# Optimization experiments

Measured on AMD Instinct MI355X. Metric: run time of the kernel, lower is better.

## Reference

```python
import jax, jax.numpy as jnp
import numpy as np
from jax import lax

EPS = 1e-8  # torch CosineSimilarity eps


def setup_inputs() -> dict:
    key = jax.random.key(0)
    k1, k2, k3 = jax.random.split(key, 3)
    B, T, D, K = 16, 2048, 768, 64
    inputs = jax.random.normal(k1, (B, T, D), dtype=jnp.float32)
    labels = jax.random.randint(k2, (B, T), 0, K, dtype=jnp.int64)
    class_avgs = jax.random.normal(k3, (K, D), dtype=jnp.float32)
    return {"inputs": inputs, "labels": labels, "class_avgs": class_avgs}


def _simrel(inputs, labels, class_avgs):
    B, T, D = inputs.shape
    K = class_avgs.shape[0]
    vecs = inputs.reshape(B * T, D)
    labs = labels.reshape(B * T)
    class_ids = jnp.arange(K)

    def step(carry, xl):
        avgs, counts = carry  # [K,D], [K]
        vec, lab = xl  # [D], scalar int
        is_inf = jnp.any(jnp.isinf(avgs), axis=1)  # [K] unseen-class flag
        vn = jnp.maximum(jnp.linalg.norm(vec), EPS)
        an = jnp.maximum(jnp.linalg.norm(avgs, axis=1), EPS)  # [K]
        cos = (avgs @ vec) / (an * vn)  # [K]
        onehot = class_ids == lab
        # unseen class: sim = 1 (cos(vec,vec)) if labeled, else -1
        sim = jnp.where(is_inf, jnp.where(onehot, 1.0, -1.0), cos)
        # training update: running mean of labeled class (counts reset per forward)
        cnt = counts[lab]
        new_row = jnp.where(is_inf[lab], vec, (avgs[lab] * cnt + vec) / (cnt + 1.0))
        avgs = avgs.at[lab].set(new_row)
        counts = counts.at[lab].add(1.0)
        return (avgs, counts), sim

    init = (class_avgs, jnp.zeros((K,), dtype=inputs.dtype))
    (_, _), sims = lax.scan(step, init, (vecs, labs))
    return sims.reshape(B, T, K)


def reference(inputs, labels, class_avgs):
    return _simrel(inputs, labels, class_avgs)
```

## Files before the change

kernel.cpp:

```cpp
#include <hip/hip_runtime.h>
#include <cstddef>

#define K 64
#define D 768
#define D4 192

__device__ __forceinline__ float d4f(float4 a, float4 b) {
  return a.x*b.x + a.y*b.y + a.z*b.z + a.w*b.w;
}
__device__ __forceinline__ float4 a4(float4 a, float4 b) {
  return make_float4(a.x+b.x, a.y+b.y, a.z+b.z, a.w+b.w);
}
__device__ __forceinline__ unsigned short f2bf(float x) {
  unsigned int u = __float_as_uint(x);
  unsigned int r = (u + 0x7FFFu + ((u >> 16) & 1u)) >> 16;
  return (unsigned short)r;
}
__device__ __forceinline__ float bflo(unsigned u) { return __uint_as_float(u << 16); }
__device__ __forceinline__ float bfhi(unsigned u) { return __uint_as_float(u & 0xFFFF0000u); }

typedef __attribute__((ext_vector_type(8)))  short bf16x8;
typedef __attribute__((ext_vector_type(16))) float f32x16;

#define NCF 256
#define CF  128
#define NF  32768

#define LDT3 68
#define LDM  136
__global__ __launch_bounds__(256) void k2_v11(
    const float* __restrict__ inputs, const int* __restrict__ labels,
    const float* __restrict__ cavg, unsigned short* __restrict__ cavgb,
    float* __restrict__ cn2,
    unsigned short* __restrict__ sums, int* __restrict__ cnts_t)
{
  __shared__ unsigned short Vt[128 * LDT3];
  __shared__ unsigned short Mt[64 * LDM];
  __shared__ int hist[64];
  const int bi = blockIdx.x;
  const int tid = threadIdx.x;

  if (bi >= NCF * 12) {
    int wave = (bi - NCF * 12) * 4 + (tid >> 6);
    int l = tid & 63;
    if (wave >= K) return;
    const float* src = cavg + (size_t)wave * D;
    unsigned short* dst = cavgb + (size_t)wave * D;
    float sq = 0.f;
#pragma unroll
    for (int t = 0; t < 3; ++t) {
      float4 v = ((const float4*)src)[t * 64 + l];
      sq += v.x*v.x + v.y*v.y + v.z*v.z + v.w*v.w;
      ushort4 o; o.x = f2bf(v.x); o.y = f2bf(v.y); o.z = f2bf(v.z); o.w = f2bf(v.w);
      ((ushort4*)dst)[t * 64 + l] = o;
    }
#pragma unroll
    for (int mm = 1; mm <= 32; mm <<= 1) sq += __shfl_xor(sq, mm);
    if (l == 0) cn2[wave] = sq;
    return;
  }

  const int m = bi / 12, g = bi % 12;
  const int w = tid >> 6, l = tid & 63;
  const int r31 = l & 31, kh = l >> 5;
  const int ch = w & 1;
  const int cw = w >> 1;

  float4 fr[8];
#pragma unroll
  for (int it = 0; it < 8; ++it) {
    int flat = it * 256 + tid;
    int row = flat >> 4, c4 = flat & 15;
    fr[it] = *(const float4*)(inputs + (size_t)(m * 128 + row) * D + g * 64 + c4 * 4);
  }

  for (int e = tid; e < 64 * LDM / 2; e += 256) ((unsigned int*)Mt)[e] = 0u;
  if (tid < 64) hist[tid] = 0;
  __syncthreads();
  if (tid < 128) {
    int lab = labels[m * 128 + tid];
    Mt[lab * LDM + tid] = 0x3F80;
    if (g == 0) atomicAdd(&hist[lab], 1);
  }
  __syncthreads();
  if (g == 0 && tid < 64) cnts_t[tid * NCF + m] = hist[tid];

#pragma unroll
  for (int it = 0; it < 8; ++it) {
    int flat = it * 256 + tid;
    int row = flat >> 4, c4 = flat & 15;
    ushort4 o;
    o.x = f2bf(fr[it].x); o.y = f2bf(fr[it].y);
    o.z = f2bf(fr[it].z); o.w = f2bf(fr[it].w);
    *(ushort4*)(Vt + row * LDT3 + c4 * 4) = o;
  }
  __syncthreads();

  f32x16 acc = (f32x16){};
#pragma unroll
  for (int kk = 0; kk < 8; ++kk) {
    bf16x8 a = *(const bf16x8*)(Mt + (ch * 32 + r31) * LDM + kk * 16 + kh * 8);
    bf16x8 b;
#pragma unroll
    for (int r = 0; r < 8; ++r)
      b[r] = *(const short*)(Vt + (kk * 16 + kh * 8 + r) * LDT3 + cw * 32 + r31);
    acc = __builtin_amdgcn_mfma_f32_32x32x16_bf16(a, b, acc, 0, 0, 0);
  }

  __syncthreads();
  unsigned short* So = Vt;
#pragma unroll
  for (int q = 0; q < 16; ++q) {
    int kc = (q & 3) + 8 * (q >> 2) + 4 * kh;
    So[(ch * 32 + kc) * 64 + cw * 32 + r31] = f2bf(acc[q]);
  }
  __syncthreads();
  unsigned short* sp = sums + (size_t)m * (K * D) + g * 64;
#pragma unroll
  for (int it = 0; it < 2; ++it) {
    int flat = it * 256 + tid;
    int row = flat >> 3, c = flat & 7;
    *(uint4*)(sp + (size_t)row * D + c * 8) = *(const uint4*)(So + row * 64 + c * 8);
  }
}

__global__ __launch_bounds__(256) void k3a_scan_lo(
    unsigned short* __restrict__ sums, float* __restrict__ aux)
{
  const int g  = blockIdx.x / 96;
  const int cp = (blockIdx.x % 96) * 256 + threadIdx.x;
  const int col = cp * 2;
  float run0 = 0.f, run1 = 0.f;
  for (int m = g * 16; m < g * 16 + 16; ++m) {
    size_t idx = (size_t)m * (K * D) + col;
    unsigned u = *(const unsigned*)(sums + idx);
    float t0 = bflo(u), t1 = bfhi(u);
    *(unsigned*)(sums + idx) = (unsigned)f2bf(run0) | ((unsigned)f2bf(run1) << 16);
    run0 += t0; run1 += t1;
  }
  aux[(size_t)g * (K * D) + col]     = run0;
  aux[(size_t)g * (K * D) + col + 1] = run1;
}

__global__ __launch_bounds__(256) void k3b_plus(
    float* __restrict__ aux, int* __restrict__ cnts_t)
{
  if (blockIdx.x == 192) {
    if (threadIdx.x < K) {
      int k = threadIdx.x;
      int run = 0;
      int* p = cnts_t + k * NCF;
      for (int mm = 0; mm < NCF; ++mm) { int t = p[mm]; p[mm] = run; run += t; }
    }
    return;
  }
  int col = blockIdx.x * 256 + threadIdx.x;
  float run = 0.f;
  for (int g = 0; g < 16; ++g) {
    size_t idx = (size_t)g * (K * D) + col;
    float t = aux[idx]; aux[idx] = run; run += t;
  }
}

#define LDV2 136
#define LDD  132
#define BUFW (2 * 128 * LDV2)
__global__ __launch_bounds__(1024, 4) void k4_v8(
    const float* __restrict__ inputs, const unsigned short* __restrict__ base,
    const float* __restrict__ aux, const unsigned short* __restrict__ cavgb,
    const int* __restrict__ labels, const int* __restrict__ cnts_t,
    const float* __restrict__ cn2, float* __restrict__ out)
{
  __shared__ unsigned short smem[2 * BUFW];
  __shared__ float pvL[128];
  __shared__ float bn2L[64];
  __shared__ int   labL[128];
  __shared__ float segA[16][64];
  __shared__ float segF[16][64];
  __shared__ float segP[16][64];
  __shared__ int   segH[16][64];
  const int m = blockIdx.x;
  const int g = m >> 4;
  const int tid = threadIdx.x;
  const int w = tid >> 6, l = tid & 63;
  const int r31 = l & 31, kh = l >> 5;
  const int wr = w & 3;
  const int wc = w >> 2;

  if (tid < 128) labL[tid] = labels[m * 128 + tid];
  if (tid < 64) bn2L[tid] = 0.f;
  __syncthreads();

  f32x16 accP = (f32x16){}, accS = (f32x16){};

  float4 vregf[4];
  uint4 breg, creg;
  float4 areg[2];

#define PREF(sx) do {                                                          \
    _Pragma("unroll")                                                          \
    for (int it = 0; it < 4; ++it) {                                           \
      int flat = it * 1024 + tid;                                              \
      int row = flat >> 5, c4 = flat & 31;                                     \
      vregf[it] = *(const float4*)(inputs + (size_t)(m * 128 + row) * D + (sx) * 128 + c4 * 4); \
    }                                                                          \
    _Pragma("unroll")                                                          \
    for (int it = 0; it < 2; ++it) {                                           \
      int flat = it * 1024 + tid;                                              \
      int row = flat >> 4, c = flat & 15;                                      \
      if (it == 0) {                                                           \
        breg = *(const uint4*)(base + ((size_t)m * K + row) * D + (sx) * 128 + c * 8); \
        const float* ap = aux + ((size_t)g * K + row) * D + (sx) * 128 + c * 8; \
        areg[0] = *(const float4*)ap;                                          \
        areg[1] = *(const float4*)(ap + 4);                                    \
      } else {                                                                 \
        creg = *(const uint4*)(cavgb + (size_t)(row - 64) * D + (sx) * 128 + c * 8); \
      }                                                                        \
    }                                                                          \
  } while (0)

#define WRITEB(pb) do {                                                        \
    unsigned short* Vt_ = smem + (pb) * BUFW;                                  \
    unsigned short* Bt_ = Vt_ + 128 * LDV2;                                    \
    _Pragma("unroll")                                                          \
    for (int it = 0; it < 4; ++it) {                                           \
      int flat = it * 1024 + tid;                                              \
      int row = flat >> 5, c4 = flat & 31;                                     \
      ushort4 o;                                                               \
      o.x = f2bf(vregf[it].x); o.y = f2bf(vregf[it].y);                        \
      o.z = f2bf(vregf[it].z); o.w = f2bf(vregf[it].w);                        \
      *(ushort4*)(Vt_ + row * LDV2 + c4 * 4) = o;                              \
    }                                                                          \
    _Pragma("unroll")                                                          \
    for (int it = 0; it < 2; ++it) {                                           \
      int flat = it * 1024 + tid;                                              \
      int row = flat >> 4, c = flat & 15;                                      \
      if (it == 0) {                                                           \
        uint4 ub = breg;                                                       \
        float4 af0 = areg[0], af1 = areg[1];                                   \
        float f0 = bflo(ub.x) + af0.x, f1 = bfhi(ub.x) + af0.y;                \
        float f2 = bflo(ub.y) + af0.z, f3 = bfhi(ub.y) + af0.w;                \
        float f4 = bflo(ub.z) + af1.x, f5 = bfhi(ub.z) + af1.y;                \
        float f6 = bflo(ub.w) + af1.z, f7 = bfhi(ub.w) + af1.w;                \
        float sq = f0*f0 + f1*f1 + f2*f2 + f3*f3 + f4*f4 + f5*f5 + f6*f6 + f7*f7; \
        sq += __shfl_xor(sq, 1); sq += __shfl_xor(sq, 2);                      \
        sq += __shfl_xor(sq, 4); sq += __shfl_xor(sq, 8);                      \
        if ((l & 15) == 0) atomicAdd(&bn2L[row], sq);                          \
        uint4 u;                                                               \
        u.x = (unsigned)f2bf(f0) | ((unsigned)f2bf(f1) << 16);                 \
        u.y = (unsigned)f2bf(f2) | ((unsigned)f2bf(f3) << 16);                 \
        u.z = (unsigned)f2bf(f4) | ((unsigned)f2bf(f5) << 16);                 \
        u.w = (unsigned)f2bf(f6) | ((unsigned)f2bf(f7) << 16);                 \
        *(uint4*)(Bt_ + row * LDV2 + c * 8) = u;                               \
      } else {                                                                 \
        *(uint4*)(Bt_ + row * LDV2 + c * 8) = creg;                            \
      }                                                                        \
    }                                                                          \
  } while (0)

  PREF(0);
  WRITEB(0);
  PREF(1);
  __syncthreads();

  for (int s = 0; s < 6; ++s) {
    const int pb = s & 1;
    if (s < 5) WRITEB(pb ^ 1);
    if (s < 4) PREF(s + 2);
    const unsigned short* Vt = smem + pb * BUFW;
    const unsigned short* Bt = Vt + 128 * LDV2;
#pragma unroll
    for (int kk = 0; kk < 8; ++kk) {
      bf16x8 av = *(const bf16x8*)(Vt + (32 * wr + r31) * LDV2 + kk * 16 + kh * 8);
      bf16x8 bB = *(const bf16x8*)(Bt + (32 * wc + r31) * LDV2 + kk * 16 + kh * 8);
      accP = __builtin_amdgcn_mfma_f32_32x32x16_bf16(av, bB, accP, 0, 0, 0);
      if (wc <= wr) {
        bf16x8 bV = *(const bf16x8*)(Vt + (32 * wc + r31) * LDV2 + kk * 16 + kh * 8);
        accS = __builtin_amdgcn_mfma_f32_32x32x16_bf16(av, bV, accS, 0, 0, 0);
      }
    }
    __syncthreads();
  }
#undef PREF
#undef WRITEB

  if (wr == wc && ((r31 >> 2) & 1) == kh) {
    int q = (r31 & 3) + 4 * (r31 >> 3);
    pvL[32 * wr + r31] = accS[q];
  }

  {
    unsigned short* Vt = smem;
    unsigned short* Bt = smem + 128 * LDV2;
#pragma unroll
    for (int q = 0; q < 16; ++q) {
      int i = 32 * wr + (q & 3) + 8 * (q >> 2) + 4 * kh;
      int j = 32 * wc + r31;
      Vt[i * LDV2 + j] = (j < i) ? f2bf(accS[q]) : (unsigned short)0;
    }
    int j = tid & 127;
    int lab = labL[j];
    int kb = (tid >> 7) * 8;
#pragma unroll
    for (int kk = 0; kk < 8; ++kk) {
      int k = kb + kk;
      Bt[k * LDV2 + j] = (lab == k) ? (unsigned short)0x3F80 : (unsigned short)0;
    }
  }
  __syncthreads();

  if (w < 8) {
    const unsigned short* Vt = smem;
    const unsigned short* Bt = smem + 128 * LDV2;
#pragma unroll
    for (int kk = 0; kk < 8; ++kk) {
      bf16x8 aS = *(const bf16x8*)(Vt + (32 * wr + r31) * LDV2 + kk * 16 + kh * 8);
      bf16x8 bM = *(const bf16x8*)(Bt + (32 * wc + r31) * LDV2 + kk * 16 + kh * 8);
      accP = __builtin_amdgcn_mfma_f32_32x32x16_bf16(aS, bM, accP, 0, 0, 0);
    }
  }
  __syncthreads();

  float* dotL = (float*)smem;
#pragma unroll
  for (int q = 0; q < 16; ++q) {
    int i = 32 * wr + (q & 3) + 8 * (q >> 2) + 4 * kh;
    dotL[i * LDD + 32 * wc + r31] = accP[q];
  }
  __syncthreads();

  {
    int k = l;
    float A = 0.f, Fv = 0.f, Pv = 0.f;
    int has = 0;
    int jb = w * 8;
    for (int j = jb; j < jb + 8; ++j) {
      if (labL[j] == k) {
        float t = 2.f * dotL[j * LDD + k] + pvL[j];
        A += t;
        if (!has) { Fv = t; Pv = pvL[j]; has = 1; }
      }
    }
    segA[w][k] = A; segF[w][k] = Fv; segP[w][k] = Pv; segH[w][k] = has;
  }
  __syncthreads();

  {
    int k = l;
    bool seen = cnts_t[k * NCF + m] > 0;
    float n = seen ? bn2L[k] : 0.f;
    for (int ww = 0; ww < w; ++ww) {
      if (segH[ww][k]) {
        n = seen ? (n + segA[ww][k])
                 : (segP[ww][k] + segA[ww][k] - segF[ww][k]);
        seen = true;
      }
    }
    float cnk = cn2[k];
    int jb = w * 8;
    for (int j = jb; j < jb + 8; ++j) {
      float dS = dotL[j * LDD + k];
      float dC = dotL[j * LDD + 64 + k];
      float pvj = pvL[j];
      int lab = labL[j];
      float val = seen ? dS : dC;
      float nn  = seen ? n : cnk;
      out[(size_t)(m * 128 + j) * K + k] = val * rsqrtf(fmaxf(nn * pvj, 1e-30f));
      if (lab == k) {
        n = seen ? (n + 2.f * dS + pvj) : pvj;
        seen = true;
      }
    }
  }
}

__global__ __launch_bounds__(256) void ph1_chunk_sums(
    const float* __restrict__ inputs, const int* __restrict__ labels,
    float* __restrict__ sums, int* __restrict__ cnts, int NC, int C)
{
  __shared__ float acc[4 * K * 64];
  __shared__ int   hist[4 * K];
  const int bi    = blockIdx.x;
  const int chunk = bi / 12, slice = bi % 12;
  const int w = threadIdx.x >> 6, l = threadIdx.x & 63;

  for (int e = threadIdx.x; e < 4 * K * 64; e += 256) acc[e] = 0.f;
  hist[threadIdx.x] = 0;
  __syncthreads();

  const int C4 = C >> 2;
  const long long rbase = (long long)chunk * C + (long long)w * C4;
  float* accw = acc + w * (K * 64);
  for (int j = 0; j < C4; ++j) {
    long long r = rbase + j;
    int lab = labels[r];
    float v = inputs[r * D + slice * 64 + l];
    accw[lab * 64 + l] += v;
    if (slice == 0 && l == 0) hist[w * K + lab]++;
  }
  __syncthreads();

  float* sp = sums + (long long)chunk * (K * D) + slice * 64;
  for (int e = threadIdx.x; e < K * 64; e += 256) {
    int k = e >> 6, dl = e & 63;
    float s = acc[0*K*64 + e] + acc[1*K*64 + e] + acc[2*K*64 + e] + acc[3*K*64 + e];
    sp[k * D + dl] = s;
  }
  if (slice == 0 && threadIdx.x < K) {
    cnts[chunk * K + threadIdx.x] =
        hist[0*K + threadIdx.x] + hist[1*K + threadIdx.x] +
        hist[2*K + threadIdx.x] + hist[3*K + threadIdx.x];
  }
}

__global__ __launch_bounds__(256) void ph2a_scan_sums(float* __restrict__ sums, int NC)
{
  const int tid = blockIdx.x * 256 + threadIdx.x;
  float run = 0.f;
  for (int m = 0; m < NC; ++m) {
    long long idx = (long long)m * (K * D) + tid;
    float t = sums[idx];
    sums[idx] = run;
    run += t;
  }
}

__global__ void ph2b_scan_cnts(int* __restrict__ cnts, int NC)
{
  const int k = threadIdx.x;
  int run = 0;
  for (int m = 0; m < NC; ++m) {
    int t = cnts[m * K + k];
    cnts[m * K + k] = run;
    run += t;
  }
}

__global__ __launch_bounds__(256, 4) void ph3_scan(
    const float* __restrict__ inputs, const int* __restrict__ labels,
    const float* __restrict__ cavg, const float* __restrict__ base,
    const int* __restrict__ cnts, float* __restrict__ out, int NC, int C)
{
  const int bi = blockIdx.x;
  int chunk, quad;
  if (NC >= 8) {
    int xcd = bi & 7, slot = bi >> 3;
    chunk = xcd * (NC >> 3) + (slot >> 2);
    quad  = slot & 3;
  } else {
    chunk = bi >> 2; quad = bi & 3;
  }
  const int w = threadIdx.x >> 6, l = threadIdx.x & 63;
  const int k0 = (quad * 4 + w) * 4;

  const int cb = chunk * K + k0;
  bool vg0 = (cnts[cb+0] == 0), vg1 = (cnts[cb+1] == 0);
  bool vg2 = (cnts[cb+2] == 0), vg3 = (cnts[cb+3] == 0);

  const float4* bp = (const float4*)base + (long long)chunk * (K * D4);
  const float4* cp = (const float4*)cavg;

  float4 A0[3], A1[3], A2[3], A3[3];
#pragma unroll
  for (int t = 0; t < 3; ++t) {
    int o = t * 64 + l;
    A0[t] = vg0 ? cp[(k0+0)*D4 + o] : bp[(k0+0)*D4 + o];
    A1[t] = vg1 ? cp[(k0+1)*D4 + o] : bp[(k0+1)*D4 + o];
    A2[t] = vg2 ? cp[(k0+2)*D4 + o] : bp[(k0+2)*D4 + o];
    A3[t] = vg3 ? cp[(k0+3)*D4 + o] : bp[(k0+3)*D4 + o];
  }
  float n0 = 0.f, n1 = 0.f, n2 = 0.f, n3 = 0.f;
#pragma unroll
  for (int t = 0; t < 3; ++t) {
    n0 += d4f(A0[t], A0[t]); n1 += d4f(A1[t], A1[t]);
    n2 += d4f(A2[t], A2[t]); n3 += d4f(A3[t], A3[t]);
  }
#pragma unroll
  for (int m = 1; m <= 32; m <<= 1) {
    n0 += __shfl_xor(n0, m); n1 += __shfl_xor(n1, m);
    n2 += __shfl_xor(n2, m); n3 += __shfl_xor(n3, m);
  }

  const long long ibase = (long long)chunk * C;
  for (int j = 0; j < C; ++j) {
    const long long i = ibase + j;
    const int lab = labels[i];
    const float4* vp = (const float4*)inputs + i * D4;
    float4 v0 = vp[l], v1 = vp[64 + l], v2 = vp[128 + l];

    float p0 = d4f(A0[0], v0) + d4f(A0[1], v1) + d4f(A0[2], v2);
    float p1 = d4f(A1[0], v0) + d4f(A1[1], v1) + d4f(A1[2], v2);
    float p2 = d4f(A2[0], v0) + d4f(A2[1], v1) + d4f(A2[2], v2);
    float p3 = d4f(A3[0], v0) + d4f(A3[1], v1) + d4f(A3[2], v2);
    float pv = d4f(v0, v0) + d4f(v1, v1) + d4f(v2, v2);
#pragma unroll
    for (int m = 1; m <= 32; m <<= 1) {
      p0 += __shfl_xor(p0, m); p1 += __shfl_xor(p1, m);
      p2 += __shfl_xor(p2, m); p3 += __shfl_xor(p3, m);
      pv += __shfl_xor(pv, m);
    }
    if (l < 4) {
      float ps = (l == 0) ? p0 : (l == 1) ? p1 : (l == 2) ? p2 : p3;
      float ns = (l == 0) ? n0 : (l == 1) ? n1 : (l == 2) ? n2 : n3;
      out[i * K + k0 + l] = ps * rsqrtf(fmaxf(ns * pv, 1e-30f));
    }
#define UPD(idx) do { \
      if (vg##idx) { A##idx[0]=v0; A##idx[1]=v1; A##idx[2]=v2; n##idx = pv; vg##idx = false; } \
      else { A##idx[0]=a4(A##idx[0],v0); A##idx[1]=a4(A##idx[1],v1); A##idx[2]=a4(A##idx[2],v2); \
             n##idx += 2.f * p##idx + pv; } } while (0)
    if      (lab == k0 + 0) UPD(0);
    else if (lab == k0 + 1) UPD(1);
    else if (lab == k0 + 2) UPD(2);
    else if (lab == k0 + 3) UPD(3);
#undef UPD
  }
}

extern "C" void kernel_launch(void* const* d_in, const int* in_sizes, int n_in,
                              void* d_out, int out_size, void* d_ws, size_t ws_size,
                              hipStream_t stream)
{
  const float* inputs = (const float*)d_in[0];
  const int*   labels = (const int*)d_in[1];
  const float* cavg   = (const float*)d_in[2];
  float* out = (float*)d_out;
  const int N = in_sizes[1];

  const size_t szSums  = (size_t)NCF * K * D * 2;
  const size_t szAux   = (size_t)16 * K * D * 4;
  const size_t szCnt   = (size_t)K * NCF * 4;
  const size_t szCavgb = (size_t)K * D * 2;
  const size_t szCn2   = (size_t)K * 4;
  size_t need = szSums + szAux + szCnt + szCavgb + szCn2 + 8 * 256;

  if (N == NF && in_sizes[2] == K * D && ws_size >= need) {
    char* p = (char*)d_ws;
    auto take = [&](size_t b) { char* r = p; p += (b + 255) & ~(size_t)255; return r; };
    unsigned short* sums  = (unsigned short*)take(szSums);
    float*          aux   = (float*)take(szAux);
    int*            cnts  = (int*)take(szCnt);
    unsigned short* cavgb = (unsigned short*)take(szCavgb);
    float*          cn2   = (float*)take(szCn2);

    hipLaunchKernelGGL(k2_v11, dim3(NCF * 12 + 16), dim3(256), 0, stream,
                       inputs, labels, cavg, cavgb, cn2, sums, cnts);
    hipLaunchKernelGGL(k3a_scan_lo, dim3(16 * 96), dim3(256), 0, stream, sums, aux);
    hipLaunchKernelGGL(k3b_plus, dim3(193), dim3(256), 0, stream, aux, cnts);
    hipLaunchKernelGGL(k4_v8, dim3(NCF), dim3(1024), 0, stream,
                       inputs, sums, aux, cavgb, labels, cnts, cn2, out);
    return;
  }

  int NC = 256;
  while (NC > 1) {
    size_t nd = (size_t)NC * K * D * 4 + (size_t)NC * K * 4;
    if (nd <= ws_size && (N % (NC * 4)) == 0) break;
    NC >>= 1;
  }
  const int C = N / NC;
  float* d_sums = (float*)d_ws;
  int*   d_cnts = (int*)((char*)d_ws + (size_t)NC * K * D * 4);

  hipLaunchKernelGGL(ph1_chunk_sums, dim3(NC * 12), dim3(256), 0, stream,
                     inputs, labels, d_sums, d_cnts, NC, C);
  hipLaunchKernelGGL(ph2a_scan_sums, dim3((K * D) / 256), dim3(256), 0, stream,
                     d_sums, NC);
  hipLaunchKernelGGL(ph2b_scan_cnts, dim3(1), dim3(64), 0, stream,
                     d_cnts, NC);
  hipLaunchKernelGGL(ph3_scan, dim3(NC * 4), dim3(256), 0, stream,
                     inputs, labels, cavg, d_sums, d_cnts, out, NC, C);
}
```

Baseline: 72.71 us.

## Split fused GEMM+epilogue kernel into two-half GEMM blocks and separate epilogue

```diff
diff --git a/kernel.cpp b/kernel.cpp
--- a/kernel.cpp
+++ b/kernel.cpp
@@ -163,15 +163,162 @@
 }
 
 #define LDV2 136
-#define LDD  132
-#define BUFW (2 * 128 * LDV2)
-__global__ __launch_bounds__(1024, 4) void k4_v8(
+#define LDS2 136
+__global__ __launch_bounds__(512, 4) void k4a_gemm(
     const float* __restrict__ inputs, const unsigned short* __restrict__ base,
     const float* __restrict__ aux, const unsigned short* __restrict__ cavgb,
-    const int* __restrict__ labels, const int* __restrict__ cnts_t,
-    const float* __restrict__ cn2, float* __restrict__ out)
-{
-  __shared__ unsigned short smem[2 * BUFW];
+    const int* __restrict__ labels,
+    float* __restrict__ dotb, float* __restrict__ pvb, float* __restrict__ bn2b)
+{
+  __shared__ unsigned short smem[2 * 128 * LDV2];
+  __shared__ float bn2L[64];
+  __shared__ int   labL[128];
+  unsigned short* Vt = smem;
+  unsigned short* Bt = smem + 128 * LDV2;
+  const int bi = blockIdx.x;
+  const int m = bi >> 1, h = bi & 1;
+  const int g = m >> 4;
+  const int tid = threadIdx.x;
+  const int w = tid >> 6, l = tid & 63;
+  const int r31 = l & 31, kh = l >> 5;
+  const int wrg = 2 * h + (w & 1);
+  const int wc  = w >> 1;
+
+  if (tid < 128) labL[tid] = labels[m * 128 + tid];
+  if (tid < 64) bn2L[tid] = 0.f;
+
+  f32x16 accP = (f32x16){}, accS = (f32x16){};
+
+  float4 vregf[8];
+  uint4 breg[2], creg[2];
+  float4 areg[4];
+
+#define PREF(sx) do {                                                          \
+    _Pragma("unroll")                                                          \
+    for (int it = 0; it < 8; ++it) {                                           \
+      int flat = it * 512 + tid;                                               \
+      int row = flat >> 5, c4 = flat & 31;                                     \
+      vregf[it] = *(const float4*)(inputs + (size_t)(m * 128 + row) * D + (sx) * 128 + c4 * 4); \
+    }                                                                          \
+    _Pragma("unroll")                                                          \
+    for (int it = 0; it < 2; ++it) {                                           \
+      int flat = it * 512 + tid;                                               \
+      int row = flat >> 4, c = flat & 15;                                      \
+      breg[it] = *(const uint4*)(base + ((size_t)m * K + row) * D + (sx) * 128 + c * 8); \
+      const float* ap = aux + ((size_t)g * K + row) * D + (sx) * 128 + c * 8;  \
+      areg[it * 2]     = *(const float4*)ap;                                   \
+      areg[it * 2 + 1] = *(const float4*)(ap + 4);                             \
+      creg[it] = *(const uint4*)(cavgb + (size_t)row * D + (sx) * 128 + c * 8);\
+    }                                                                          \
+  } while (0)
+
+#define WRITEB() do {                                                          \
+    _Pragma("unroll")                                                          \
+    for (int it = 0; it < 8; ++it) {                                           \
+      int flat = it * 512 + tid;                                               \
+      int row = flat >> 5, c4 = flat & 31;                                     \
+      ushort4 o;                                                               \
+      o.x = f2bf(vregf[it].x); o.y = f2bf(vregf[it].y);                        \
+      o.z = f2bf(vregf[it].z); o.w = f2bf(vregf[it].w);                        \
+      *(ushort4*)(Vt + row * LDV2 + c4 * 4) = o;                               \
+    }                                                                          \
+    _Pragma("unroll")                                                          \
+    for (int it = 0; it < 2; ++it) {                                           \
+      int flat = it * 512 + tid;                                               \
+      int row = flat >> 4, c = flat & 15;                                      \
+      uint4 ub = breg[it];                                                     \
+      float4 af0 = areg[it * 2], af1 = areg[it * 2 + 1];                       \
+      float f0 = bflo(ub.x) + af0.x, f1 = bfhi(ub.x) + af0.y;                  \
+      float f2 = bflo(ub.y) + af0.z, f3 = bfhi(ub.y) + af0.w;                  \
+      float f4 = bflo(ub.z) + af1.x, f5 = bfhi(ub.z) + af1.y;                  \
+      float f6 = bflo(ub.w) + af1.z, f7 = bfhi(ub.w) + af1.w;                  \
+      float sq = f0*f0 + f1*f1 + f2*f2 + f3*f3 + f4*f4 + f5*f5 + f6*f6 + f7*f7;\
+      sq += __shfl_xor(sq, 1); sq += __shfl_xor(sq, 2);                        \
+      sq += __shfl_xor(sq, 4); sq += __shfl_xor(sq, 8);                        \
+      if ((l & 15) == 0) atomicAdd(&bn2L[row], sq);                            \
+      uint4 u;                                                                 \
+      u.x = (unsigned)f2bf(f0) | ((unsigned)f2bf(f1) << 16);                   \
+      u.y = (unsigned)f2bf(f2) | ((unsigned)f2bf(f3) << 16);                   \
+      u.z = (unsigned)f2bf(f4) | ((unsigned)f2bf(f5) << 16);                   \
+      u.w = (unsigned)f2bf(f6) | ((unsigned)f2bf(f7) << 16);                   \
+      *(uint4*)(Bt + row * LDV2 + c * 8) = u;                                  \
+      *(uint4*)(Bt + (64 + row) * LDV2 + c * 8) = creg[it];                    \
+    }                                                                          \
+  } while (0)
+
+  PREF(0);
+
+  for (int s = 0; s < 6; ++s) {
+    __syncthreads();
+    WRITEB();
+    if (s < 5) PREF(s + 1);
+    __syncthreads();
+#pragma unroll
+    for (int kk = 0; kk < 8; ++kk) {
+      bf16x8 av = *(const bf16x8*)(Vt + (32 * wrg + r31) * LDV2 + kk * 16 + kh * 8);
+      bf16x8 bB = *(const bf16x8*)(Bt + (32 * wc + r31) * LDV2 + kk * 16 + kh * 8);
+      accP = __builtin_amdgcn_mfma_f32_32x32x16_bf16(av, bB, accP, 0, 0, 0);
+      if (wc <= wrg) {
+        bf16x8 bV = *(const bf16x8*)(Vt + (32 * wc + r31) * LDV2 + kk * 16 + kh * 8);
+        accS = __builtin_amdgcn_mfma_f32_32x32x16_bf16(av, bV, accS, 0, 0, 0);
+      }
+    }
+  }
+#undef PREF
+#undef WRITEB
+
+  if (wc == wrg && ((r31 >> 2) & 1) == kh) {
+    int q = (r31 & 3) + 4 * (r31 >> 3);
+    pvb[(size_t)m * 128 + 32 * wrg + r31] = accS[q];
+  }
+  __syncthreads();
+  if (h == 0 && tid < 64) bn2b[m * 64 + tid] = bn2L[tid];
+
+  unsigned short* SL  = smem;
+  unsigned short* MtL = smem + 64 * LDS2;
+  __syncthreads();
+#pragma unroll
+  for (int q = 0; q < 16; ++q) {
+    int i_loc = 32 * (w & 1) + (q & 3) + 8 * (q >> 2) + 4 * kh;
+    int i_glob = 64 * h + i_loc;
+    int j = 32 * wc + r31;
+    SL[i_loc * LDS2 + j] = (j < i_glob) ? f2bf(accS[q]) : (unsigned short)0;
+  }
+  {
+    int j = tid & 127;
+    int lab = labL[j];
+    int kb = (tid >> 7) * 16;
+#pragma unroll
+    for (int kk = 0; kk < 16; ++kk) {
+      int k = kb + kk;
+      MtL[k * LDS2 + j] = (lab == k) ? (unsigned short)0x3F80 : (unsigned short)0;
+    }
+  }
+  __syncthreads();
+
+  if (w < 4) {
+#pragma unroll
+    for (int kk = 0; kk < 8; ++kk) {
+      bf16x8 aS = *(const bf16x8*)(SL + (32 * (w & 1) + r31) * LDS2 + kk * 16 + kh * 8);
+      bf16x8 bM = *(const bf16x8*)(MtL + (32 * (w >> 1) + r31) * LDS2 + kk * 16 + kh * 8);
+      accP = __builtin_amdgcn_mfma_f32_32x32x16_bf16(aS, bM, accP, 0, 0, 0);
+    }
+  }
+
+#pragma unroll
+  for (int q = 0; q < 16; ++q) {
+    int i_glob = 32 * wrg + (q & 3) + 8 * (q >> 2) + 4 * kh;
+    int col = 32 * wc + r31;
+    dotb[((size_t)m * 128 + i_glob) * 128 + col] = accP[q];
+  }
+}
+
+__global__ __launch_bounds__(1024) void k5_ep(
+    const float* __restrict__ dotb, const float* __restrict__ pvb,
+    const float* __restrict__ bn2b, const int* __restrict__ labels,
+    const int* __restrict__ cnts_t, const float* __restrict__ cn2,
+    float* __restrict__ out)
+{
   __shared__ float pvL[128];
   __shared__ float bn2L[64];
   __shared__ int   labL[128];
@@ -180,154 +327,14 @@
   __shared__ float segP[16][64];
   __shared__ int   segH[16][64];
   const int m = blockIdx.x;
-  const int g = m >> 4;
   const int tid = threadIdx.x;
   const int w = tid >> 6, l = tid & 63;
-  const int r31 = l & 31, kh = l >> 5;
-  const int wr = w & 3;
-  const int wc = w >> 2;
-
-  if (tid < 128) labL[tid] = labels[m * 128 + tid];
-  if (tid < 64) bn2L[tid] = 0.f;
-  __syncthreads();
-
-  f32x16 accP = (f32x16){}, accS = (f32x16){};
-
-  float4 vregf[4];
-  uint4 breg, creg;
-  float4 areg[2];
-
-#define PREF(sx) do {                                                          \
-    _Pragma("unroll")                                                          \
-    for (int it = 0; it < 4; ++it) {                                           \
-      int flat = it * 1024 + tid;                                              \
-      int row = flat >> 5, c4 = flat & 31;                                     \
-      vregf[it] = *(const float4*)(inputs + (size_t)(m * 128 + row) * D + (sx) * 128 + c4 * 4); \
-    }                                                                          \
-    _Pragma("unroll")                                                          \
-    for (int it = 0; it < 2; ++it) {                                           \
-      int flat = it * 1024 + tid;                                              \
-      int row = flat >> 4, c = flat & 15;                                      \
-      if (it == 0) {                                                           \
-        breg = *(const uint4*)(base + ((size_t)m * K + row) * D + (sx) * 128 + c * 8); \
-        const float* ap = aux + ((size_t)g * K + row) * D + (sx) * 128 + c * 8; \
-        areg[0] = *(const float4*)ap;                                          \
-        areg[1] = *(const float4*)(ap + 4);                                    \
-      } else {                                                                 \
-        creg = *(const uint4*)(cavgb + (size_t)(row - 64) * D + (sx) * 128 + c * 8); \
-      }                                                                        \
-    }                                                                          \
-  } while (0)
-
-#define WRITEB(pb) do {                                                        \
-    unsigned short* Vt_ = smem + (pb) * BUFW;                                  \
-    unsigned short* Bt_ = Vt_ + 128 * LDV2;                                    \
-    _Pragma("unroll")                                                          \
-    for (int it = 0; it < 4; ++it) {                                           \
-      int flat = it * 1024 + tid;                                              \
-      int row = flat >> 5, c4 = flat & 31;                                     \
-      ushort4 o;                                                               \
-      o.x = f2bf(vregf[it].x); o.y = f2bf(vregf[it].y);                        \
-      o.z = f2bf(vregf[it].z); o.w = f2bf(vregf[it].w);                        \
-      *(ushort4*)(Vt_ + row * LDV2 + c4 * 4) = o;                              \
-    }                                                                          \
-    _Pragma("unroll")                                                          \
-    for (int it = 0; it < 2; ++it) {                                           \
-      int flat = it * 1024 + tid;                                              \
-      int row = flat >> 4, c = flat & 15;                                      \
-      if (it == 0) {                                                           \
-        uint4 ub = breg;                                                       \
-        float4 af0 = areg[0], af1 = areg[1];                                   \
-        float f0 = bflo(ub.x) + af0.x, f1 = bfhi(ub.x) + af0.y;                \
-        float f2 = bflo(ub.y) + af0.z, f3 = bfhi(ub.y) + af0.w;                \
-        float f4 = bflo(ub.z) + af1.x, f5 = bfhi(ub.z) + af1.y;                \
-        float f6 = bflo(ub.w) + af1.z, f7 = bfhi(ub.w) + af1.w;                \
-        float sq = f0*f0 + f1*f1 + f2*f2 + f3*f3 + f4*f4 + f5*f5 + f6*f6 + f7*f7; \
-        sq += __shfl_xor(sq, 1); sq += __shfl_xor(sq, 2);                      \
-        sq += __shfl_xor(sq, 4); sq += __shfl_xor(sq, 8);                      \
-        if ((l & 15) == 0) atomicAdd(&bn2L[row], sq);                          \
-        uint4 u;                                                               \
-        u.x = (unsigned)f2bf(f0) | ((unsigned)f2bf(f1) << 16);                 \
-        u.y = (unsigned)f2bf(f2) | ((unsigned)f2bf(f3) << 16);                 \
-        u.z = (unsigned)f2bf(f4) | ((unsigned)f2bf(f5) << 16);                 \
-        u.w = (unsigned)f2bf(f6) | ((unsigned)f2bf(f7) << 16);                 \
-        *(uint4*)(Bt_ + row * LDV2 + c * 8) = u;                               \
-      } else {                                                                 \
-        *(uint4*)(Bt_ + row * LDV2 + c * 8) = creg;                            \
-      }                                                                        \
-    }                                                                          \
-  } while (0)
-
-  PREF(0);
-  WRITEB(0);
-  PREF(1);
-  __syncthreads();
-
-  for (int s = 0; s < 6; ++s) {
-    const int pb = s & 1;
-    if (s < 5) WRITEB(pb ^ 1);
-    if (s < 4) PREF(s + 2);
-    const unsigned short* Vt = smem + pb * BUFW;
-    const unsigned short* Bt = Vt + 128 * LDV2;
-#pragma unroll
-    for (int kk = 0; kk < 8; ++kk) {
-      bf16x8 av = *(const bf16x8*)(Vt + (32 * wr + r31) * LDV2 + kk * 16 + kh * 8);
-      bf16x8 bB = *(const bf16x8*)(Bt + (32 * wc + r31) * LDV2 + kk * 16 + kh * 8);
-      accP = __builtin_amdgcn_mfma_f32_32x32x16_bf16(av, bB, accP, 0, 0, 0);
-      if (wc <= wr) {
-        bf16x8 bV = *(const bf16x8*)(Vt + (32 * wc + r31) * LDV2 + kk * 16 + kh * 8);
-        accS = __builtin_amdgcn_mfma_f32_32x32x16_bf16(av, bV, accS, 0, 0, 0);
-      }
-    }
-    __syncthreads();
-  }
-#undef PREF
-#undef WRITEB
-
-  if (wr == wc && ((r31 >> 2) & 1) == kh) {
-    int q = (r31 & 3) + 4 * (r31 >> 3);
-    pvL[32 * wr + r31] = accS[q];
-  }
-
-  {
-    unsigned short* Vt = smem;
-    unsigned short* Bt = smem + 128 * LDV2;
-#pragma unroll
-    for (int q = 0; q < 16; ++q) {
-      int i = 32 * wr + (q & 3) + 8 * (q >> 2) + 4 * kh;
-      int j = 32 * wc + r31;
-      Vt[i * LDV2 + j] = (j < i) ? f2bf(accS[q]) : (unsigned short)0;
-    }
-    int j = tid & 127;
-    int lab = labL[j];
-    int kb = (tid >> 7) * 8;
-#pragma unroll
-    for (int kk = 0; kk < 8; ++kk) {
-      int k = kb + kk;
-      Bt[k * LDV2 + j] = (lab == k) ? (unsigned short)0x3F80 : (unsigned short)0;
-    }
-  }
-  __syncthreads();
-
-  if (w < 8) {
-    const unsigned short* Vt = smem;
-    const unsigned short* Bt = smem + 128 * LDV2;
-#pragma unroll
-    for (int kk = 0; kk < 8; ++kk) {
-      bf16x8 aS = *(const bf16x8*)(Vt + (32 * wr + r31) * LDV2 + kk * 16 + kh * 8);
-      bf16x8 bM = *(const bf16x8*)(Bt + (32 * wc + r31) * LDV2 + kk * 16 + kh * 8);
-      accP = __builtin_amdgcn_mfma_f32_32x32x16_bf16(aS, bM, accP, 0, 0, 0);
-    }
-  }
-  __syncthreads();
-
-  float* dotL = (float*)smem;
-#pragma unroll
-  for (int q = 0; q < 16; ++q) {
-    int i = 32 * wr + (q & 3) + 8 * (q >> 2) + 4 * kh;
-    dotL[i * LDD + 32 * wc + r31] = accP[q];
-  }
-  __syncthreads();
+
+  if (tid < 128) { labL[tid] = labels[m * 128 + tid]; pvL[tid] = pvb[(size_t)m * 128 + tid]; }
+  if (tid < 64) bn2L[tid] = bn2b[m * 64 + tid];
+  __syncthreads();
+
+  const float* dm = dotb + (size_t)m * 128 * 128;
 
   {
     int k = l;
@@ -336,7 +343,7 @@
     int jb = w * 8;
     for (int j = jb; j < jb + 8; ++j) {
       if (labL[j] == k) {
-        float t = 2.f * dotL[j * LDD + k] + pvL[j];
+        float t = 2.f * dm[(size_t)j * 128 + k] + pvL[j];
         A += t;
         if (!has) { Fv = t; Pv = pvL[j]; has = 1; }
       }
@@ -359,8 +366,8 @@
     float cnk = cn2[k];
     int jb = w * 8;
     for (int j = jb; j < jb + 8; ++j) {
-      float dS = dotL[j * LDD + k];
-      float dC = dotL[j * LDD + 64 + k];
+      float dS = dm[(size_t)j * 128 + k];
+      float dC = dm[(size_t)j * 128 + 64 + k];
       float pvj = pvL[j];
       int lab = labL[j];
       float val = seen ? dS : dC;
@@ -528,16 +535,22 @@
 
   const size_t szSums  = (size_t)NCF * K * D * 2;
   const size_t szAux   = (size_t)16 * K * D * 4;
+  const size_t szDot   = (size_t)NF * 128 * 4;
+  const size_t szPvb   = (size_t)NF * 4;
+  const size_t szBn2   = (size_t)NCF * K * 4;
   const size_t szCnt   = (size_t)K * NCF * 4;
   const size_t szCavgb = (size_t)K * D * 2;
   const size_t szCn2   = (size_t)K * 4;
-  size_t need = szSums + szAux + szCnt + szCavgb + szCn2 + 8 * 256;
+  size_t need = szSums + szAux + szDot + szPvb + szBn2 + szCnt + szCavgb + szCn2 + 10 * 256;
 
   if (N == NF && in_sizes[2] == K * D && ws_size >= need) {
     char* p = (char*)d_ws;
     auto take = [&](size_t b) { char* r = p; p += (b + 255) & ~(size_t)255; return r; };
     unsigned short* sums  = (unsigned short*)take(szSums);
     float*          aux   = (float*)take(szAux);
+    float*          dotb  = (float*)take(szDot);
+    float*          pvb   = (float*)take(szPvb);
+    float*          bn2b  = (float*)take(szBn2);
     int*            cnts  = (int*)take(szCnt);
     unsigned short* cavgb = (unsigned short*)take(szCavgb);
     float*          cn2   = (float*)take(szCn2);
@@ -546,8 +559,10 @@
                        inputs, labels, cavg, cavgb, cn2, sums, cnts);
     hipLaunchKernelGGL(k3a_scan_lo, dim3(16 * 96), dim3(256), 0, stream, sums, aux);
     hipLaunchKernelGGL(k3b_plus, dim3(193), dim3(256), 0, stream, aux, cnts);
-    hipLaunchKernelGGL(k4_v8, dim3(NCF), dim3(1024), 0, stream,
-                       inputs, sums, aux, cavgb, labels, cnts, cn2, out);
+    hipLaunchKernelGGL(k4a_gemm, dim3(NCF * 2), dim3(512), 0, stream,
+                       inputs, sums, aux, cavgb, labels, dotb, pvb, bn2b);
+    hipLaunchKernelGGL(k5_ep, dim3(NCF), dim3(1024), 0, stream,
+                       dotb, pvb, bn2b, labels, cnts, cn2, out);
     return;
   }
 
```

Measured after the change: 125.3 us. +72.3%, slower.
